# Kernel tuning notes

Hardware: AMD Instinct MI355X
Metric: run time of the kernel (lower is better)

## Reference

```python
import jax, jax.numpy as jnp
import numpy as np

IN_FEATURES = 4096
OUT_FEATURES = 11008
B, S = 8, 512


def setup_inputs() -> dict:
    key = jax.random.key(0)
    k1, k2, k3 = jax.random.split(key, 3)
    x = jax.random.normal(k1, (B, S, IN_FEATURES), dtype=jnp.float32)
    # int8 weights simulated as int32 values in [-127, 127]
    weight_int8 = jax.random.randint(k2, (OUT_FEATURES, IN_FEATURES), -127, 128, dtype=jnp.int32)
    # per-output-channel scales (positive, small, like absmax/127)
    weight_scale = jax.random.uniform(k3, (OUT_FEATURES,), dtype=jnp.float32) * 0.01 + 1e-4
    return {"x": x, "weight_int8": weight_int8, "weight_scale": weight_scale}


def reference(x, weight_int8, weight_scale):
    # On-the-fly dequantization: W[o, i] = int8[o, i] * scale[o]
    weight = weight_int8.astype(x.dtype) * weight_scale.astype(x.dtype)[:, None]
    # F.linear: y = x @ W^T  -> [B, S, out_features]
    return jnp.einsum('bsi,oi->bso', x, weight)
```

## Files before the change

### kernel.cpp

```cpp
#include <hip/hip_runtime.h>
#include <stdint.h>

#define M_DIM 4096
#define N_DIM 11008
#define K_DIM 4096

typedef int i32x4 __attribute__((ext_vector_type(4)));

static __device__ __forceinline__ void direct_load16(const void* gptr, void* ldsptr) {
    __builtin_amdgcn_global_load_lds(
        (const __attribute__((address_space(1))) void*)gptr,
        (__attribute__((address_space(3))) void*)ldsptr,
        16, 0, 0);
}

__global__ __launch_bounds__(256) void cvt_w_kernel(const int* __restrict__ w,
                                                    int8_t* __restrict__ o) {
    int t = blockIdx.x * 256 + threadIdx.x;
    const int4* w4 = (const int4*)w;
    int4 a = w4[t];
    ((unsigned*)o)[t] = (a.x & 255) | ((a.y & 255) << 8) | ((a.z & 255) << 16) | (a.w << 24);
}

__global__ __launch_bounds__(256) void quant_x_kernel(const float* __restrict__ x,
                                                      int8_t* __restrict__ xq,
                                                      float* __restrict__ xs) {
    __shared__ float wmax[4];
    const int row = blockIdx.x;
    const int t = threadIdx.x;
    const float4* xr = (const float4*)(x + (size_t)row * K_DIM);

    float4 v[4];
    float am = 0.0f;
#pragma unroll
    for (int p = 0; p < 4; p++) {
        v[p] = xr[p * 256 + t];
        am = fmaxf(am, fmaxf(fmaxf(fabsf(v[p].x), fabsf(v[p].y)),
                             fmaxf(fabsf(v[p].z), fabsf(v[p].w))));
    }
#pragma unroll
    for (int o = 32; o > 0; o >>= 1)
        am = fmaxf(am, __shfl_xor(am, o));
    if ((t & 63) == 0) wmax[t >> 6] = am;
    __syncthreads();
    am = fmaxf(fmaxf(wmax[0], wmax[1]), fmaxf(wmax[2], wmax[3]));

    const float inv = 127.0f / am;
    int* oq = (int*)(xq + (size_t)row * K_DIM);
#pragma unroll
    for (int p = 0; p < 4; p++) {
        int qa = (int)rintf(v[p].x * inv);
        int qb = (int)rintf(v[p].y * inv);
        int qc = (int)rintf(v[p].z * inv);
        int qd = (int)rintf(v[p].w * inv);
        oq[p * 256 + t] = (qa & 255) | ((qb & 255) << 8) | ((qc & 255) << 16) | (qd << 24);
    }
    if (t == 0) xs[row] = am * (1.0f / 127.0f);
}


#define NT (K_DIM / 64)

__global__ __launch_bounds__(512, 2) void gemm_i8_kernel(
    const int8_t* __restrict__ A,
    const int8_t* __restrict__ B,
    const float* __restrict__ xs,
    const float* __restrict__ ws,
    float* __restrict__ C)
{
    __shared__ __align__(16) int8_t As[4][256 * 64];
    __shared__ __align__(16) int8_t Bs[4][256 * 64];

    const int tid  = threadIdx.x;
    const int lane = tid & 63;
    const int wave = tid >> 6;
    const int wm   = wave >> 2;
    const int wn   = wave & 3;
    const int quad = lane >> 4;
    const int r16  = lane & 15;

    const int orig = blockIdx.x + (blockIdx.y << 4);
    const int work = (orig & 7) * 86 + (orig >> 3);
    const int m0 = (work & 15) * 256;
    const int n0 = (work >> 4) * 256;

    const int srow   = tid >> 2;
    const int schunk = (tid & 3) ^ ((tid >> 3) & 3);
    const int8_t* gA = A + (size_t)(m0 + srow) * K_DIM + schunk * 16;
    const int8_t* gB = B + (size_t)(n0 + srow) * K_DIM + schunk * 16;
    const size_t half2 = (size_t)128 * K_DIM;
    const int wb = wave * 1024;

    const int fsw   = (r16 >> 1) & 3;
    const int a_off = (wm * 128 + r16) * 64 + ((quad ^ fsw) * 16);
    const int b_off = (wn * 64  + r16) * 64 + ((quad ^ fsw) * 16);

    i32x4 acc[8][4];
#pragma unroll
    for (int i = 0; i < 8; i++)
#pragma unroll
        for (int j = 0; j < 4; j++) acc[i][j] = (i32x4)(0);

#define STAGE(t) do {                                                        \
        char* _la = (char*)As[(t) & 3] + wb;                                 \
        char* _lb = (char*)Bs[(t) & 3] + wb;                                 \
        const size_t _ko = (size_t)(t) * 64;                                 \
        direct_load16(gA + _ko,         _la);                                \
        direct_load16(gA + _ko + half2, _la + 8192);                         \
        direct_load16(gB + _ko,         _lb);                                \
        direct_load16(gB + _ko + half2, _lb + 8192);                         \
    } while (0)

#define COMPUTE(t) do {                                                      \
        const int8_t* _as = As[(t) & 3];                                     \
        const int8_t* _bs = Bs[(t) & 3];                                     \
        i32x4 af[8], bf[4];                                                  \
        _Pragma("unroll")                                                    \
        for (int _i = 0; _i < 8; _i++)                                       \
            af[_i] = *(const i32x4*)(_as + a_off + _i * 1024);               \
        _Pragma("unroll")                                                    \
        for (int _j = 0; _j < 4; _j++)                                       \
            bf[_j] = *(const i32x4*)(_bs + b_off + _j * 1024);               \
        __builtin_amdgcn_s_setprio(1);                                       \
        _Pragma("unroll")                                                    \
        for (int _i = 0; _i < 8; _i++)                                       \
            _Pragma("unroll")                                                \
            for (int _j = 0; _j < 4; _j++)                                   \
                acc[_i][_j] = __builtin_amdgcn_mfma_i32_16x16x64_i8(         \
                    af[_i], bf[_j], acc[_i][_j], 0, 0, 0);                   \
        __builtin_amdgcn_s_setprio(0);                                       \
    } while (0)

    STAGE(0); STAGE(1); STAGE(2);
    asm volatile("s_waitcnt vmcnt(8)" ::: "memory");
    __builtin_amdgcn_s_barrier();
    asm volatile("" ::: "memory");

    for (int t = 0; t < NT - 3; ++t) {
        STAGE(t + 3);
        COMPUTE(t);
        asm volatile("s_waitcnt vmcnt(8)" ::: "memory");
        __builtin_amdgcn_s_barrier();
        asm volatile("" ::: "memory");
    }
    COMPUTE(NT - 3);
    asm volatile("s_waitcnt vmcnt(4)" ::: "memory");
    __builtin_amdgcn_s_barrier();
    asm volatile("" ::: "memory");
    COMPUTE(NT - 2);
    asm volatile("s_waitcnt vmcnt(0)" ::: "memory");
    __builtin_amdgcn_s_barrier();
    asm volatile("" ::: "memory");
    COMPUTE(NT - 1);

#undef STAGE
#undef COMPUTE

#pragma unroll
    for (int i = 0; i < 8; i++) {
        const int mrow = m0 + wm * 128 + i * 16 + quad * 4;
        float rsc[4];
#pragma unroll
        for (int r = 0; r < 4; r++) rsc[r] = xs[mrow + r];
#pragma unroll
        for (int j = 0; j < 4; j++) {
            const int n = n0 + wn * 64 + j * 16 + r16;
            const float s = ws[n];
#pragma unroll
            for (int r = 0; r < 4; r++)
                C[(size_t)(mrow + r) * N_DIM + n] = (float)acc[i][j][r] * s * rsc[r];
        }
    }
}


extern "C" void kernel_launch(void* const* d_in, const int* in_sizes, int n_in,
                              void* d_out, int out_size, void* d_ws, size_t ws_size,
                              hipStream_t stream) {
    const float* x       = (const float*)d_in[0];
    const int*   w_int   = (const int*)d_in[1];
    const float* w_scale = (const float*)d_in[2];
    float*       out     = (float*)d_out;

    int8_t* wq = (int8_t*)d_ws;
    int8_t* xq = (int8_t*)((char*)d_ws + (size_t)N_DIM * K_DIM);
    float*  xs = (float*)((char*)d_ws + (size_t)N_DIM * K_DIM + (size_t)M_DIM * K_DIM);

    cvt_w_kernel<<<dim3(N_DIM * K_DIM / 4 / 256), dim3(256), 0, stream>>>(w_int, wq);
    quant_x_kernel<<<dim3(M_DIM), dim3(256), 0, stream>>>(x, xq, xs);
    gemm_i8_kernel<<<dim3(M_DIM / 256, N_DIM / 256), dim3(512), 0, stream>>>(xq, wq, xs, w_scale, out);
}
```

Baseline: 609.6 us.

## Split each K-tile into two barrier-separated phases interleaving A/B loads with MFMA

Restructures the int8 GEMM main loop so each K-tile's compute is split into two half-phases, each issuing half of the next stage's global-to-LDS loads (A then B) between the fragment reads and the MFMA block, with extra barriers. The loop is unrolled by four over the LDS ring buffers, and the tail iterations clamp to redundant reloads of tile 63 instead of a separate epilogue. This aims to spread memory issue across compute and interleave waves more finely, at the cost of twice as many barriers and some wasted loads at the end.

```diff
diff --git a/kernel.cpp b/kernel.cpp
--- a/kernel.cpp
+++ b/kernel.cpp
@@ -59,8 +59,6 @@
 }
 
 
-#define NT (K_DIM / 64)
-
 __global__ __launch_bounds__(512, 2) void gemm_i8_kernel(
     const int8_t* __restrict__ A,
     const int8_t* __restrict__ B,
@@ -101,60 +99,63 @@
 #pragma unroll
         for (int j = 0; j < 4; j++) acc[i][j] = (i32x4)(0);
 
-#define STAGE(t) do {                                                        \
-        char* _la = (char*)As[(t) & 3] + wb;                                 \
-        char* _lb = (char*)Bs[(t) & 3] + wb;                                 \
-        const size_t _ko = (size_t)(t) * 64;                                 \
-        direct_load16(gA + _ko,         _la);                                \
-        direct_load16(gA + _ko + half2, _la + 8192);                         \
-        direct_load16(gB + _ko,         _lb);                                \
-        direct_load16(gB + _ko + half2, _lb + 8192);                         \
+#define STAGE_A(t, buf) do {                                                  \
+        direct_load16(gA + (size_t)(t) * 64,         (char*)As[buf] + wb);    \
+        direct_load16(gA + (size_t)(t) * 64 + half2, (char*)As[buf] + wb + 8192); \
+    } while (0)
+#define STAGE_B(t, buf) do {                                                  \
+        direct_load16(gB + (size_t)(t) * 64,         (char*)Bs[buf] + wb);    \
+        direct_load16(gB + (size_t)(t) * 64 + half2, (char*)Bs[buf] + wb + 8192); \
     } while (0)
 
-#define COMPUTE(t) do {                                                      \
-        const int8_t* _as = As[(t) & 3];                                     \
-        const int8_t* _bs = Bs[(t) & 3];                                     \
-        i32x4 af[8], bf[4];                                                  \
-        _Pragma("unroll")                                                    \
-        for (int _i = 0; _i < 8; _i++)                                       \
-            af[_i] = *(const i32x4*)(_as + a_off + _i * 1024);               \
-        _Pragma("unroll")                                                    \
-        for (int _j = 0; _j < 4; _j++)                                       \
-            bf[_j] = *(const i32x4*)(_bs + b_off + _j * 1024);               \
-        __builtin_amdgcn_s_setprio(1);                                       \
-        _Pragma("unroll")                                                    \
-        for (int _i = 0; _i < 8; _i++)                                       \
-            _Pragma("unroll")                                                \
-            for (int _j = 0; _j < 4; _j++)                                   \
-                acc[_i][_j] = __builtin_amdgcn_mfma_i32_16x16x64_i8(         \
-                    af[_i], bf[_j], acc[_i][_j], 0, 0, 0);                   \
-        __builtin_amdgcn_s_setprio(0);                                       \
+#define PHASE(rbuf, h, STAGE_STMT, DOVM) do {                                 \
+        const int8_t* _as = As[rbuf];                                         \
+        const int8_t* _bs = Bs[rbuf];                                         \
+        i32x4 af[4], bf[4];                                                   \
+        _Pragma("unroll")                                                     \
+        for (int _i = 0; _i < 4; _i++)                                        \
+            af[_i] = *(const i32x4*)(_as + a_off + ((h) * 4 + _i) * 1024);    \
+        _Pragma("unroll")                                                     \
+        for (int _j = 0; _j < 4; _j++)                                        \
+            bf[_j] = *(const i32x4*)(_bs + b_off + _j * 1024);                \
+        STAGE_STMT;                                                           \
+        __builtin_amdgcn_s_barrier();                                         \
+        __builtin_amdgcn_s_setprio(1);                                        \
+        _Pragma("unroll")                                                     \
+        for (int _i = 0; _i < 4; _i++)                                        \
+            _Pragma("unroll")                                                 \
+            for (int _j = 0; _j < 4; _j++)                                    \
+                acc[(h) * 4 + _i][_j] = __builtin_amdgcn_mfma_i32_16x16x64_i8(\
+                    af[_i], bf[_j], acc[(h) * 4 + _i][_j], 0, 0, 0);          \
+        __builtin_amdgcn_s_setprio(0);                                        \
+        if (DOVM) asm volatile("s_waitcnt vmcnt(8)" ::: "memory");            \
+        __builtin_amdgcn_s_barrier();                                         \
     } while (0)
 
-    STAGE(0); STAGE(1); STAGE(2);
+    STAGE_A(0, 0); STAGE_B(0, 0);
+    STAGE_A(1, 1); STAGE_B(1, 1);
+    STAGE_A(2, 2); STAGE_B(2, 2);
     asm volatile("s_waitcnt vmcnt(8)" ::: "memory");
     __builtin_amdgcn_s_barrier();
-    asm volatile("" ::: "memory");
 
-    for (int t = 0; t < NT - 3; ++t) {
-        STAGE(t + 3);
-        COMPUTE(t);
-        asm volatile("s_waitcnt vmcnt(8)" ::: "memory");
-        __builtin_amdgcn_s_barrier();
-        asm volatile("" ::: "memory");
+    for (int i = 0; i < 16; ++i) {
+        const int t3 = 4 * i + 3;
+        const int t4 = (4 * i + 4 > 63) ? 63 : 4 * i + 4;
+        const int t5 = (4 * i + 5 > 63) ? 63 : 4 * i + 5;
+        const int t6 = (4 * i + 6 > 63) ? 63 : 4 * i + 6;
+        PHASE(0, 0, STAGE_A(t3, 3), 0);
+        PHASE(0, 1, STAGE_B(t3, 3), 1);
+        PHASE(1, 0, STAGE_A(t4, 0), 0);
+        PHASE(1, 1, STAGE_B(t4, 0), 1);
+        PHASE(2, 0, STAGE_A(t5, 1), 0);
+        PHASE(2, 1, STAGE_B(t5, 1), 1);
+        PHASE(3, 0, STAGE_A(t6, 2), 0);
+        PHASE(3, 1, STAGE_B(t6, 2), 1);
     }
-    COMPUTE(NT - 3);
-    asm volatile("s_waitcnt vmcnt(4)" ::: "memory");
-    __builtin_amdgcn_s_barrier();
-    asm volatile("" ::: "memory");
-    COMPUTE(NT - 2);
-    asm volatile("s_waitcnt vmcnt(0)" ::: "memory");
-    __builtin_amdgcn_s_barrier();
-    asm volatile("" ::: "memory");
-    COMPUTE(NT - 1);
 
-#undef STAGE
-#undef COMPUTE
+#undef PHASE
+#undef STAGE_A
+#undef STAGE_B
 
 #pragma unroll
     for (int i = 0; i < 8; i++) {
```

Result: faster. 555.6 us (-8.9%).
